# Optimization experiments

Measured on AMD Instinct MI355X. Metric: run time of the kernel, lower is better.

The kernel has to match this reference:

```python
import jax, jax.numpy as jnp
import numpy as np

N = 50000
E0 = 800000
IN_CH = 128
HID = 64
OUT_CH = 64
HEADS = 2
NEG_SLOPE = 0.2


def _xavier(key, shape):
    fan_in, fan_out = shape[-2], shape[-1]
    limit = (6.0 / (fan_in + fan_out)) ** 0.5
    return jax.random.uniform(key, shape, jnp.float32, -limit, limit)


def setup_inputs() -> dict:
    key = jax.random.key(0)
    ks = jax.random.split(key, 10)
    x = jax.random.normal(ks[0], (N, IN_CH), jnp.float32)
    src = jax.random.randint(ks[1], (E0,), 0, N)
    dst = jax.random.randint(ks[2], (E0,), 0, N)
    dst = jnp.where(src == dst, (dst + 1) % N, dst)  # no self loops in input
    edge_index = jnp.stack([src, dst]).astype(jnp.int64)
    emb_w = _xavier(ks[3], (HID, IN_CH))
    emb_b = jnp.zeros((HID,), jnp.float32)
    # layer 0: in=HID, out=HID, heads=HEADS
    w0 = _xavier(ks[4], (HEADS, HID, HID))
    a0 = _xavier(ks[5], (1, HEADS, 2 * HID))
    # layer 1: in=HEADS*HID, out=HID, heads=HEADS
    w1 = _xavier(ks[6], (HEADS, HEADS * HID, HID))
    a1 = _xavier(ks[7], (1, HEADS, 2 * HID))
    # layer 2: in=HEADS*HID, out=OUT_CH, heads=1, concat=False
    w2 = _xavier(ks[8], (1, HEADS * HID, OUT_CH))
    a2 = _xavier(ks[9], (1, 1, 2 * OUT_CH))
    return {"x": x, "edge_index": edge_index, "emb_w": emb_w, "emb_b": emb_b,
            "w0": w0, "a0": a0, "w1": w1, "a1": a1, "w2": w2, "a2": a2}


def gat_layer(x, w, a, src, dst, concat):
    # x: [N, F_in]; w: [H, F_in, C]; a: [1, H, 2C]; src/dst: [E]
    C = w.shape[-1]
    xh = jnp.einsum('nf,hfc->nhc', x, w)               # [N, H, C]
    a_i, a_j = a[0, :, :C], a[0, :, C:]                # each [H, C]
    # (cat(x_i, x_j) * a).sum(-1) == <x_i, a_i> + <x_j, a_j>; compute per node then gather
    s_i = jnp.einsum('nhc,hc->nh', xh, a_i)            # [N, H]
    s_j = jnp.einsum('nhc,hc->nh', xh, a_j)            # [N, H]
    alpha = jax.nn.leaky_relu(s_i[dst] + s_j[src], NEG_SLOPE)  # [E, H]
    # segment softmax over destination nodes
    m = jax.ops.segment_max(alpha, dst, num_segments=N)
    alpha = jnp.exp(alpha - m[dst])
    denom = jax.ops.segment_sum(alpha, dst, num_segments=N)
    alpha = alpha / (denom[dst] + 1e-16)
    out = jax.ops.segment_sum(xh[src] * alpha[:, :, None], dst, num_segments=N)  # [N, H, C]
    if concat:
        return out.reshape(N, -1)
    return out.mean(axis=1)


def _forward(x, edge_index, emb_w, emb_b, w0, a0, w1, a1, w2, a2):
    # add self loops (inputs contain none, matching remove+add in the source)
    loop = jnp.arange(N, dtype=edge_index.dtype)
    src = jnp.concatenate([edge_index[0], loop])
    dst = jnp.concatenate([edge_index[1], loop])
    h = x @ emb_w.T + emb_b                            # nn.Linear embedding
    h = jax.nn.elu(gat_layer(h, w0, a0, src, dst, True))
    h = jax.nn.elu(gat_layer(h, w1, a1, src, dst, True))
    h = jax.nn.elu(gat_layer(h, w2, a2, src, dst, False))
    return h


def reference(x, edge_index, emb_w, emb_b, w0, a0, w1, a1, w2, a2):
    return _forward(x, edge_index, emb_w, emb_b, w0, a0, w1, a1, w2, a2)
```

## Files before the change

### kernel.cpp

```cpp
#include <hip/hip_runtime.h>
#include <math.h>

typedef __attribute__((ext_vector_type(8))) short short8v;
typedef __attribute__((ext_vector_type(4))) float float4v;

union uf32 { unsigned int u; float f; };

__device__ __forceinline__ unsigned short f2b(float f) {
  uf32 v; v.f = f;
  unsigned int u = v.u;
  return (unsigned short)((u + 0x7fffu + ((u >> 16) & 1u)) >> 16);
}

__global__ void zero8(int* __restrict__ p, int n) {
  int i = blockIdx.x * 256 + threadIdx.x;
  if (i < n) p[i] = 0;
}

__global__ void hist8(const int* __restrict__ ei, int* __restrict__ cnt8,
                      unsigned short* __restrict__ lpos, int E0, int N) {
  int e = blockIdx.x * 256 + threadIdx.x;
  if (e >= E0 + N) return;
  int vx = blockIdx.x & 7;
  int d = (e < E0) ? ei[E0 + e] : (e - E0);
  lpos[e] = (unsigned short)atomicAdd(&cnt8[vx * N + d], 1);
}

__global__ void fold8(const int* __restrict__ cnt8, int* __restrict__ base8,
                      int* __restrict__ cnt, int* __restrict__ part, int N) {
  __shared__ int lds[256];
  int d = blockIdx.x * 256 + threadIdx.x;
  int run = 0;
  if (d < N) {
#pragma unroll
    for (int x = 0; x < 8; ++x) {
      int t = cnt8[x * N + d];
      base8[x * N + d] = run;
      run += t;
    }
    cnt[d] = run;
  }
  lds[threadIdx.x] = (d < N) ? run : 0;
  __syncthreads();
  for (int o = 128; o; o >>= 1) {
    if (threadIdx.x < o) lds[threadIdx.x] += lds[threadIdx.x + o];
    __syncthreads();
  }
  if (threadIdx.x == 0) part[blockIdx.x] = lds[0];
}

__global__ void scan_carry(int* __restrict__ part, int nb) {
  __shared__ int lds[256];
  __shared__ int carry;
  if (threadIdx.x == 0) carry = 0;
  __syncthreads();
  for (int t0 = 0; t0 < nb; t0 += 256) {
    int t = t0 + threadIdx.x;
    int v = (t < nb) ? part[t] : 0;
    lds[threadIdx.x] = v;
    __syncthreads();
    for (int o = 1; o < 256; o <<= 1) {
      int x = (threadIdx.x >= o) ? lds[threadIdx.x - o] : 0;
      __syncthreads();
      lds[threadIdx.x] += x;
      __syncthreads();
    }
    if (t < nb) part[t] = carry + lds[threadIdx.x] - v;
    __syncthreads();
    if (threadIdx.x == 255) carry += lds[255];
    __syncthreads();
  }
}

__global__ void scan3(const int* __restrict__ cnt, const int* __restrict__ part,
                      const int* __restrict__ base8, int* __restrict__ rp,
                      int* __restrict__ rb8, int N, int E) {
  __shared__ int lds[256];
  int t = threadIdx.x;
  int idx = blockIdx.x * 256 + t;
  int v = (idx < N) ? cnt[idx] : 0;
  lds[t] = v;
  __syncthreads();
  for (int o = 1; o < 256; o <<= 1) {
    int x = (t >= o) ? lds[t - o] : 0;
    __syncthreads();
    lds[t] += x;
    __syncthreads();
  }
  if (idx < N) {
    const int rpv = part[blockIdx.x] + lds[t] - v;
    rp[idx] = rpv;
#pragma unroll
    for (int x = 0; x < 8; ++x) rb8[x * N + idx] = rpv + base8[x * N + idx];
  }
  if (blockIdx.x == 0 && t == 0) rp[N] = E;
}

__global__ void fillx(const int* __restrict__ ei, const int* __restrict__ rb8,
                      const unsigned short* __restrict__ lpos,
                      int* __restrict__ col, int E0, int N) {
  int e = blockIdx.x * 256 + threadIdx.x;
  if (e >= E0 + N) return;
  int vx = blockIdx.x & 7;
  int s, d;
  if (e < E0) { s = ei[e]; d = ei[E0 + e]; }
  else        { s = e - E0; d = s; }
  col[rb8[vx * N + d] + lpos[e]] = s;
}

__global__ void pack_all(const float* __restrict__ emb_w, const float* __restrict__ w0,
                         const float* __restrict__ w1, const float* __restrict__ w2,
                         unsigned short* __restrict__ pE, unsigned short* __restrict__ p0,
                         unsigned short* __restrict__ p1, unsigned short* __restrict__ p2) {
  int b = blockIdx.x;
  const float* w; unsigned short* bp;
  int F, sf, sc, h;
  if (b < 32)       { w = emb_w; bp = pE; F = 128; sf = 1;  sc = 128; h = 0; }
  else if (b < 64)  { b -= 32;  w = w0; bp = p0; F = 64;  sf = 64; sc = 1; h = b / 16; b %= 16; }
  else if (b < 128) { b -= 64;  w = w1; bp = p1; F = 128; sf = 64; sc = 1; h = b / 32; b %= 32; }
  else              { b -= 128; w = w2; bp = p2; F = 128; sf = 64; sc = 1; h = 0; }
  int i = b * 256 + threadIdx.x;
  if (i >= F * 64) return;
  int j = i & 7, colc = (i >> 3) & 15, g = (i >> 7) & 3, ct = (i >> 9) & 3, kk = i >> 11;
  int f = kk * 32 + g * 8 + j;
  int c = ct * 16 + colc;
  float v = w[(size_t)h * F * 64 + (size_t)f * sf + (size_t)c * sc];
  bp[(size_t)h * F * 64 + i] = f2b(v);
}

__global__ __launch_bounds__(256) void gemm_emb_l0(
    const float* __restrict__ x, const unsigned short* __restrict__ packE,
    const float* __restrict__ emb_b, const unsigned short* __restrict__ pack0,
    const float* __restrict__ a0, unsigned short* __restrict__ xhb,
    float* __restrict__ si, float* __restrict__ sj, int nrows) {
  constexpr int SA = 136;
  constexpr int SB = 72;
  __shared__ __align__(16) unsigned short lds[64 * SA];

  const int tid = threadIdx.x;
  const int lane = tid & 63;
  const int wv = tid >> 6;
  const int n0 = blockIdx.x * 64;

#pragma unroll
  for (int i0 = 0; i0 < 64 * 32; i0 += 256) {
    const int i = i0 + tid;
    const int row = i >> 5, c4 = i & 31;
    int rg = n0 + row;
    if (rg >= nrows) rg = nrows - 1;
    const float4 v = *reinterpret_cast<const float4*>(x + (size_t)rg * 128 + c4 * 4);
    unsigned short* d = lds + row * SA + c4 * 4;
    d[0] = f2b(v.x); d[1] = f2b(v.y); d[2] = f2b(v.z); d[3] = f2b(v.w);
  }
  __syncthreads();

  const int g = lane >> 4;
  const int cl = lane & 15;

  short8v xf[4];
  {
    const unsigned short* ar = lds + (wv * 16 + cl) * SA + g * 8;
#pragma unroll
    for (int kk = 0; kk < 4; ++kk) xf[kk] = *reinterpret_cast<const short8v*>(ar + kk * 32);
  }

  float4v eacc[4];
#pragma unroll
  for (int ct = 0; ct < 4; ++ct) eacc[ct] = (float4v){0.f, 0.f, 0.f, 0.f};
#pragma unroll
  for (int kk = 0; kk < 4; ++kk) {
#pragma unroll
    for (int ct = 0; ct < 4; ++ct) {
      const short8v bf = *reinterpret_cast<const short8v*>(
          packE + ((size_t)((kk * 4 + ct) * 4 + g)) * 128 + cl * 8);
      eacc[ct] = __builtin_amdgcn_mfma_f32_16x16x32_bf16(xf[kk], bf, eacc[ct], 0, 0, 0);
    }
  }
  __syncthreads();

#pragma unroll
  for (int ct = 0; ct < 4; ++ct) {
    const float b = emb_b[ct * 16 + cl];
#pragma unroll
    for (int reg = 0; reg < 4; ++reg) {
      const int row = wv * 16 + g * 4 + reg;
      lds[row * SB + ct * 16 + cl] = f2b(eacc[ct][reg] + b);
    }
  }
  __syncthreads();

  short8v af[2];
  {
    const unsigned short* ar2 = lds + (wv * 16 + cl) * SB + g * 8;
#pragma unroll
    for (int kk = 0; kk < 2; ++kk) af[kk] = *reinterpret_cast<const short8v*>(ar2 + kk * 32);
  }

#pragma unroll
  for (int h = 0; h < 2; ++h) {
    const unsigned short* __restrict__ bph = pack0 + (size_t)h * (64 * 64);

    float4v acc[4];
#pragma unroll
    for (int ct = 0; ct < 4; ++ct) acc[ct] = (float4v){0.f, 0.f, 0.f, 0.f};
#pragma unroll
    for (int kk = 0; kk < 2; ++kk) {
#pragma unroll
      for (int ct = 0; ct < 4; ++ct) {
        const short8v bf = *reinterpret_cast<const short8v*>(
            bph + ((size_t)((kk * 4 + ct) * 4 + g)) * 128 + cl * 8);
        acc[ct] = __builtin_amdgcn_mfma_f32_16x16x32_bf16(af[kk], bf, acc[ct], 0, 0, 0);
      }
    }

#pragma unroll
    for (int ct = 0; ct < 4; ++ct) {
      const int c = ct * 16 + cl;
#pragma unroll
      for (int reg = 0; reg < 4; ++reg) {
        const int n = n0 + wv * 16 + g * 4 + reg;
        if (n < nrows) xhb[(size_t)n * 128 + h * 64 + c] = f2b(acc[ct][reg]);
      }
    }

    float pi[4] = {0.f, 0.f, 0.f, 0.f}, pj[4] = {0.f, 0.f, 0.f, 0.f};
#pragma unroll
    for (int ct = 0; ct < 4; ++ct) {
      const float av = a0[h * 128 + ct * 16 + cl];
      const float bv = a0[h * 128 + 64 + ct * 16 + cl];
#pragma unroll
      for (int reg = 0; reg < 4; ++reg) {
        pi[reg] = fmaf(acc[ct][reg], av, pi[reg]);
        pj[reg] = fmaf(acc[ct][reg], bv, pj[reg]);
      }
    }
#pragma unroll
    for (int reg = 0; reg < 4; ++reg) {
#pragma unroll
      for (int o = 8; o; o >>= 1) {
        pi[reg] += __shfl_xor(pi[reg], o, 64);
        pj[reg] += __shfl_xor(pj[reg], o, 64);
      }
    }
    if (cl == 0) {
#pragma unroll
      for (int reg = 0; reg < 4; ++reg) {
        const int n = n0 + wv * 16 + g * 4 + reg;
        if (n < nrows) {
          si[(size_t)n * 2 + h] = pi[reg];
          sj[(size_t)n * 2 + h] = pj[reg];
        }
      }
    }
  }
}

template <int F, int H, bool SCORES, bool OBF>
__global__ __launch_bounds__(256) void gemm_mfma(
    const unsigned short* __restrict__ in, const unsigned short* __restrict__ bp,
    const float* __restrict__ a, void* __restrict__ xh_out,
    float* __restrict__ si, float* __restrict__ sj, int nrows) {
  constexpr int SA = F + 8;
  constexpr int NK = F / 32;
  constexpr int HC = H * 64;
  __shared__ __align__(16) unsigned short A_lds[64 * SA];

  const int tid = threadIdx.x;
  const int lane = tid & 63;
  const int wv = tid >> 6;
  const int n0 = blockIdx.x * 64;

  {
    constexpr int NCH = 64 * F / 8;
#pragma unroll
    for (int i0 = 0; i0 < NCH; i0 += 256) {
      const int i = i0 + tid;
      const int row = i / (F / 8);
      const int c8 = i % (F / 8);
      int rg = n0 + row;
      if (rg >= nrows) rg = nrows - 1;
      const short8v v = *reinterpret_cast<const short8v*>(in + (size_t)rg * F + c8 * 8);
      *reinterpret_cast<short8v*>(A_lds + row * SA + c8 * 8) = v;
    }
  }
  __syncthreads();

  const int g = lane >> 4;
  const int cl = lane & 15;

  short8v af[NK];
  const unsigned short* ar = A_lds + (wv * 16 + cl) * SA + g * 8;
#pragma unroll
  for (int kk = 0; kk < NK; ++kk) af[kk] = *reinterpret_cast<const short8v*>(ar + kk * 32);

#pragma unroll
  for (int h = 0; h < H; ++h) {
    const unsigned short* __restrict__ bph = bp + (size_t)h * (F * 64);

    float4v acc[4];
#pragma unroll
    for (int ct = 0; ct < 4; ++ct) acc[ct] = (float4v){0.f, 0.f, 0.f, 0.f};

#pragma unroll
    for (int kk = 0; kk < NK; ++kk) {
#pragma unroll
      for (int ct = 0; ct < 4; ++ct) {
        const short8v bf = *reinterpret_cast<const short8v*>(
            bph + ((size_t)((kk * 4 + ct) * 4 + g)) * 128 + cl * 8);
        acc[ct] = __builtin_amdgcn_mfma_f32_16x16x32_bf16(af[kk], bf, acc[ct], 0, 0, 0);
      }
    }

#pragma unroll
    for (int ct = 0; ct < 4; ++ct) {
      const int c = ct * 16 + cl;
#pragma unroll
      for (int reg = 0; reg < 4; ++reg) {
        const int n = n0 + wv * 16 + g * 4 + reg;
        if (n < nrows) {
          const size_t idx = (size_t)n * HC + h * 64 + c;
          if (OBF) ((unsigned short*)xh_out)[idx] = f2b(acc[ct][reg]);
          else     ((float*)xh_out)[idx] = acc[ct][reg];
        }
      }
    }

    if (SCORES) {
      float pi[4] = {0.f, 0.f, 0.f, 0.f}, pj[4] = {0.f, 0.f, 0.f, 0.f};
#pragma unroll
      for (int ct = 0; ct < 4; ++ct) {
        const float av = a[h * 128 + ct * 16 + cl];
        const float bv = a[h * 128 + 64 + ct * 16 + cl];
#pragma unroll
        for (int reg = 0; reg < 4; ++reg) {
          pi[reg] = fmaf(acc[ct][reg], av, pi[reg]);
          pj[reg] = fmaf(acc[ct][reg], bv, pj[reg]);
        }
      }
#pragma unroll
      for (int reg = 0; reg < 4; ++reg) {
#pragma unroll
        for (int o = 8; o; o >>= 1) {
          pi[reg] += __shfl_xor(pi[reg], o, 64);
          pj[reg] += __shfl_xor(pj[reg], o, 64);
        }
      }
      if (cl == 0) {
#pragma unroll
        for (int reg = 0; reg < 4; ++reg) {
          const int n = n0 + wv * 16 + g * 4 + reg;
          if (n < nrows) {
            si[(size_t)n * H + h] = pi[reg];
            sj[(size_t)n * H + h] = pj[reg];
          }
        }
      }
    }
  }
}

template <int H, bool OBF>
__global__ __launch_bounds__(256) void agg_kernel(
    const unsigned short* __restrict__ xh, const float* __restrict__ si_g,
    const float* __restrict__ sj_g, const int* __restrict__ rp,
    const int* __restrict__ col, void* __restrict__ out, int N) {
  constexpr int HC = H * 64;
  const int lane = threadIdx.x & 63;
  const int n = blockIdx.x * 4 + (threadIdx.x >> 6);
  if (n >= N) return;
  const int el = lane & 31;
  const int hl = (H == 2) ? (lane >> 5) : 0;

  const int base = rp[n];
  const int deg = rp[n + 1] - base;
  const float siv = si_g[(size_t)n * H + hl];

  const int soff = (H == 1) ? (lane >> 5) : 0;
  const int qoff = (H == 1) ? (lane >> 5) : (lane & 32);
  constexpr int STEP = (H == 2) ? 1 : 2;
  const unsigned int loff = (H == 2) ? (unsigned)lane * 2 : (unsigned)el * 2;

  float m = 0.f, den = 0.f, acc0 = 0.f, acc1 = 0.f;

  for (int start = 0; start < deg; start += 32) {
    const int k = start + el;
    const bool vld = k < deg;
    const int s = vld ? col[base + k] : 0;
    float al = -INFINITY;
    if (vld) {
      const float t = siv + sj_g[(size_t)s * H + hl];
      al = (t > 0.f) ? t : 0.2f * t;
    }
    float cm = al;
#pragma unroll
    for (int o = 16; o; o >>= 1) cm = fmaxf(cm, __shfl_xor(cm, o, 64));
    if (start == 0) {
      m = cm;
    } else {
      const float nm = fmaxf(m, cm);
      const float r = __expf(m - nm);
      den *= r; acc0 *= r; acc1 *= r; m = nm;
    }
    const float p = vld ? __expf(al - m) : 0.f;
    float ps = p;
#pragma unroll
    for (int o = 16; o; o >>= 1) ps += __shfl_xor(ps, o, 64);
    den += ps;

    const int cc = min(32, deg - start);
    int kk = 0;
    for (; kk + 8 * STEP <= cc; kk += 8 * STEP) {
      int sb[8]; float qb[8]; unsigned int uv[8];
#pragma unroll
      for (int u = 0; u < 8; ++u) {
        const int e = kk + u * STEP;
        sb[u] = __shfl(s, e + soff, 64);
        qb[u] = __shfl(p, e + qoff, 64);
      }
#pragma unroll
      for (int u = 0; u < 8; ++u)
        uv[u] = *reinterpret_cast<const unsigned int*>(xh + (size_t)sb[u] * HC + loff);
#pragma unroll
      for (int u = 0; u < 8; ++u) {
        uf32 lo, hi;
        lo.u = uv[u] << 16;
        hi.u = uv[u] & 0xffff0000u;
        acc0 = fmaf(qb[u], lo.f, acc0);
        acc1 = fmaf(qb[u], hi.f, acc1);
      }
    }
    for (; kk + 4 * STEP <= cc; kk += 4 * STEP) {
      int sb[4]; float qb[4]; unsigned int uv[4];
#pragma unroll
      for (int u = 0; u < 4; ++u) {
        const int e = kk + u * STEP;
        sb[u] = __shfl(s, e + soff, 64);
        qb[u] = __shfl(p, e + qoff, 64);
      }
#pragma unroll
      for (int u = 0; u < 4; ++u)
        uv[u] = *reinterpret_cast<const unsigned int*>(xh + (size_t)sb[u] * HC + loff);
#pragma unroll
      for (int u = 0; u < 4; ++u) {
        uf32 lo, hi;
        lo.u = uv[u] << 16;
        hi.u = uv[u] & 0xffff0000u;
        acc0 = fmaf(qb[u], lo.f, acc0);
        acc1 = fmaf(qb[u], hi.f, acc1);
      }
    }
    for (; kk < cc; kk += STEP) {
      const int sb = __shfl(s, kk + soff, 64);
      const float qb = __shfl(p, kk + qoff, 64);
      const unsigned int uv = *reinterpret_cast<const unsigned int*>(xh + (size_t)sb * HC + loff);
      uf32 lo, hi;
      lo.u = uv << 16;
      hi.u = uv & 0xffff0000u;
      acc0 = fmaf(qb, lo.f, acc0);
      acc1 = fmaf(qb, hi.f, acc1);
    }
  }

  if (H == 2) {
    const float invd = 1.f / (den + 1e-16f);
    float v0 = acc0 * invd, v1 = acc1 * invd;
    v0 = (v0 > 0.f) ? v0 : expm1f(v0);
    v1 = (v1 > 0.f) ? v1 : expm1f(v1);
    if (OBF) {
      unsigned int pk = ((unsigned int)f2b(v1) << 16) | (unsigned int)f2b(v0);
      *reinterpret_cast<unsigned int*>((unsigned short*)out + (size_t)n * 128 + lane * 2) = pk;
    } else {
      float2 o; o.x = v0; o.y = v1;
      *reinterpret_cast<float2*>((float*)out + (size_t)n * 128 + lane * 2) = o;
    }
  } else {
    acc0 += __shfl_xor(acc0, 32, 64);
    acc1 += __shfl_xor(acc1, 32, 64);
    if (lane < 32) {
      const float invd = 1.f / (den + 1e-16f);
      float v0 = acc0 * invd, v1 = acc1 * invd;
      v0 = (v0 > 0.f) ? v0 : expm1f(v0);
      v1 = (v1 > 0.f) ? v1 : expm1f(v1);
      if (OBF) {
        unsigned int pk = ((unsigned int)f2b(v1) << 16) | (unsigned int)f2b(v0);
        *reinterpret_cast<unsigned int*>((unsigned short*)out + (size_t)n * 64 + el * 2) = pk;
      } else {
        float2 o; o.x = v0; o.y = v1;
        *reinterpret_cast<float2*>((float*)out + (size_t)n * 64 + el * 2) = o;
      }
    }
  }
}

extern "C" void kernel_launch(void* const* d_in, const int* in_sizes, int n_in,
                              void* d_out, int out_size, void* d_ws, size_t ws_size,
                              hipStream_t stream) {
  const float* x     = (const float*)d_in[0];
  const int*   ei    = (const int*)d_in[1];
  const float* emb_w = (const float*)d_in[2];
  const float* emb_b = (const float*)d_in[3];
  const float* w0    = (const float*)d_in[4];
  const float* a0    = (const float*)d_in[5];
  const float* w1    = (const float*)d_in[6];
  const float* a1    = (const float*)d_in[7];
  const float* w2    = (const float*)d_in[8];
  const float* a2    = (const float*)d_in[9];

  const int IN_CH = 128;
  int N  = in_sizes[0] / IN_CH;
  int E0 = in_sizes[1] / 2;
  int E  = E0 + N;

  char* p = (char*)d_ws;
  auto alloc = [&](size_t bytes) -> char* {
    char* r = p;
    p += (bytes + 255) & ~(size_t)255;
    return r;
  };
  unsigned short* hA  = (unsigned short*)alloc((size_t)N * 128 * 2);
  unsigned short* hB  = (unsigned short*)alloc((size_t)N * 128 * 2);
  unsigned short* xhb = (unsigned short*)alloc((size_t)N * 128 * 2);
  float* si   = (float*)alloc((size_t)N * 2 * 4);
  float* sj   = (float*)alloc((size_t)N * 2 * 4);
  unsigned short* packE = (unsigned short*)alloc(128 * 64 * 2);
  unsigned short* pack0 = (unsigned short*)alloc(2 * 64 * 64 * 2);
  unsigned short* pack1 = (unsigned short*)alloc(2 * 128 * 64 * 2);
  unsigned short* pack2 = (unsigned short*)alloc(128 * 64 * 2);
  int* rp    = (int*)alloc((size_t)(N + 1) * 4);
  int* cnt   = (int*)alloc((size_t)N * 4);
  int* cnt8  = (int*)alloc((size_t)8 * N * 4);
  int* base8 = (int*)alloc((size_t)8 * N * 4);
  int* rb8   = (int*)alloc((size_t)8 * N * 4);
  unsigned short* lpos = (unsigned short*)alloc((size_t)E * 2);
  int* col   = (int*)alloc((size_t)E * 4);
  int* part  = (int*)alloc(1024);

  dim3 blk(256);
  int gN = (N + 255) / 256;
  int gE = (E + 255) / 256;

  zero8<<<(8 * N + 255) / 256, blk, 0, stream>>>(cnt8, 8 * N);
  hist8<<<gE, blk, 0, stream>>>(ei, cnt8, lpos, E0, N);
  fold8<<<gN, blk, 0, stream>>>(cnt8, base8, cnt, part, N);
  scan_carry<<<1, blk, 0, stream>>>(part, gN);
  scan3<<<gN, blk, 0, stream>>>(cnt, part, base8, rp, rb8, N, E);
  fillx<<<gE, blk, 0, stream>>>(ei, rb8, lpos, col, E0, N);

  pack_all<<<160, blk, 0, stream>>>(emb_w, w0, w1, w2, packE, pack0, pack1, pack2);

  int gR = (N + 63) / 64;

  gemm_emb_l0<<<gR, blk, 0, stream>>>(x, packE, emb_b, pack0, a0, xhb, si, sj, N);
  agg_kernel<2, true><<<(N + 3) / 4, blk, 0, stream>>>(xhb, si, sj, rp, col, hB, N);

  gemm_mfma<128, 2, true, true><<<gR, blk, 0, stream>>>(hB, pack1, a1, xhb, si, sj, N);
  agg_kernel<2, true><<<(N + 3) / 4, blk, 0, stream>>>(xhb, si, sj, rp, col, hA, N);

  gemm_mfma<128, 1, true, true><<<gR, blk, 0, stream>>>(hA, pack2, a2, xhb, si, sj, N);
  agg_kernel<1, false><<<(N + 3) / 4, blk, 0, stream>>>(xhb, si, sj, rp, col, (float*)d_out, N);
}
```

Baseline: 201.7 us.

## Drop running softmax max and gather several edges per wave with 8-byte loads

The aggregation kernel no longer keeps a running max for the segment softmax. It takes exp of the leaky-relu score clamped at 75, and sums the denominator per lane with a single reduction at the end. This removes the per-chunk max shuffles and the rescaling of the accumulators. The gather is also reorganised so each lane loads 4 bf16 values (uint2) and half- or quarter-waves handle different edges at once, with a cross-lane reduction before the ELU and the store. The max-free exp assumes scores stay in a moderate range; very negative scores for every neighbour could underflow the denominator, and scores above 75 are clipped.

Result: no change. 205.6 us (+1.9%).

```diff
diff --git a/kernel.cpp b/kernel.cpp
--- a/kernel.cpp
+++ b/kernel.cpp
@@ -375,119 +375,96 @@
   const int deg = rp[n + 1] - base;
   const float siv = si_g[(size_t)n * H + hl];
 
-  const int soff = (H == 1) ? (lane >> 5) : 0;
-  const int qoff = (H == 1) ? (lane >> 5) : (lane & 32);
-  constexpr int STEP = (H == 2) ? 1 : 2;
-  const unsigned int loff = (H == 2) ? (unsigned)lane * 2 : (unsigned)el * 2;
-
-  float m = 0.f, den = 0.f, acc0 = 0.f, acc1 = 0.f;
+  const int egrp = (H == 2) ? (lane >> 5) : (lane >> 4);
+  constexpr int STEP = (H == 2) ? 2 : 4;
+  const int qsrc = (H == 2) ? (egrp + ((lane & 16) << 1)) : egrp;
+  const unsigned short* xrow = xh + ((H == 2) ? (unsigned)(lane & 31) * 4
+                                              : (unsigned)(lane & 15) * 4);
+
+  float den_l = 0.f;
+  float a0 = 0.f, a1 = 0.f, a2 = 0.f, a3 = 0.f;
 
   for (int start = 0; start < deg; start += 32) {
     const int k = start + el;
     const bool vld = k < deg;
     const int s = vld ? col[base + k] : 0;
-    float al = -INFINITY;
+    float p = 0.f;
     if (vld) {
       const float t = siv + sj_g[(size_t)s * H + hl];
-      al = (t > 0.f) ? t : 0.2f * t;
-    }
-    float cm = al;
-#pragma unroll
-    for (int o = 16; o; o >>= 1) cm = fmaxf(cm, __shfl_xor(cm, o, 64));
-    if (start == 0) {
-      m = cm;
-    } else {
-      const float nm = fmaxf(m, cm);
-      const float r = __expf(m - nm);
-      den *= r; acc0 *= r; acc1 *= r; m = nm;
-    }
-    const float p = vld ? __expf(al - m) : 0.f;
-    float ps = p;
-#pragma unroll
-    for (int o = 16; o; o >>= 1) ps += __shfl_xor(ps, o, 64);
-    den += ps;
+      const float al = (t > 0.f) ? t : 0.2f * t;
+      p = __expf(fminf(al, 75.f));
+    }
+    den_l += p;
 
     const int cc = min(32, deg - start);
     int kk = 0;
-    for (; kk + 8 * STEP <= cc; kk += 8 * STEP) {
-      int sb[8]; float qb[8]; unsigned int uv[8];
-#pragma unroll
-      for (int u = 0; u < 8; ++u) {
-        const int e = kk + u * STEP;
-        sb[u] = __shfl(s, e + soff, 64);
-        qb[u] = __shfl(p, e + qoff, 64);
-      }
-#pragma unroll
-      for (int u = 0; u < 8; ++u)
-        uv[u] = *reinterpret_cast<const unsigned int*>(xh + (size_t)sb[u] * HC + loff);
-#pragma unroll
-      for (int u = 0; u < 8; ++u) {
-        uf32 lo, hi;
-        lo.u = uv[u] << 16;
-        hi.u = uv[u] & 0xffff0000u;
-        acc0 = fmaf(qb[u], lo.f, acc0);
-        acc1 = fmaf(qb[u], hi.f, acc1);
-      }
-    }
     for (; kk + 4 * STEP <= cc; kk += 4 * STEP) {
-      int sb[4]; float qb[4]; unsigned int uv[4];
+      int sb[4]; float qb[4]; uint2 uv[4];
 #pragma unroll
       for (int u = 0; u < 4; ++u) {
         const int e = kk + u * STEP;
-        sb[u] = __shfl(s, e + soff, 64);
-        qb[u] = __shfl(p, e + qoff, 64);
+        sb[u] = __shfl(s, e + egrp, 64);
+        qb[u] = __shfl(p, e + qsrc, 64);
       }
 #pragma unroll
       for (int u = 0; u < 4; ++u)
-        uv[u] = *reinterpret_cast<const unsigned int*>(xh + (size_t)sb[u] * HC + loff);
+        uv[u] = *reinterpret_cast<const uint2*>(xrow + (size_t)sb[u] * HC);
 #pragma unroll
       for (int u = 0; u < 4; ++u) {
-        uf32 lo, hi;
-        lo.u = uv[u] << 16;
-        hi.u = uv[u] & 0xffff0000u;
-        acc0 = fmaf(qb[u], lo.f, acc0);
-        acc1 = fmaf(qb[u], hi.f, acc1);
+        uf32 f0, f1, f2, f3;
+        f0.u = uv[u].x << 16; f1.u = uv[u].x & 0xffff0000u;
+        f2.u = uv[u].y << 16; f3.u = uv[u].y & 0xffff0000u;
+        a0 = fmaf(qb[u], f0.f, a0);
+        a1 = fmaf(qb[u], f1.f, a1);
+        a2 = fmaf(qb[u], f2.f, a2);
+        a3 = fmaf(qb[u], f3.f, a3);
       }
     }
     for (; kk < cc; kk += STEP) {
-      const int sb = __shfl(s, kk + soff, 64);
-      const float qb = __shfl(p, kk + qoff, 64);
-      const unsigned int uv = *reinterpret_cast<const unsigned int*>(xh + (size_t)sb * HC + loff);
-      uf32 lo, hi;
-      lo.u = uv << 16;
-      hi.u = uv & 0xffff0000u;
-      acc0 = fmaf(qb, lo.f, acc0);
-      acc1 = fmaf(qb, hi.f, acc1);
-    }
-  }
-
-  if (H == 2) {
+      const int sb = __shfl(s, kk + egrp, 64);
+      const float qb = __shfl(p, kk + qsrc, 64);
+      const uint2 uv = *reinterpret_cast<const uint2*>(xrow + (size_t)sb * HC);
+      uf32 f0, f1, f2, f3;
+      f0.u = uv.x << 16; f1.u = uv.x & 0xffff0000u;
+      f2.u = uv.y << 16; f3.u = uv.y & 0xffff0000u;
+      a0 = fmaf(qb, f0.f, a0);
+      a1 = fmaf(qb, f1.f, a1);
+      a2 = fmaf(qb, f2.f, a2);
+      a3 = fmaf(qb, f3.f, a3);
+    }
+  }
+
+  a0 += __shfl_xor(a0, 32, 64);
+  a1 += __shfl_xor(a1, 32, 64);
+  a2 += __shfl_xor(a2, 32, 64);
+  a3 += __shfl_xor(a3, 32, 64);
+  if (H == 1) {
+    a0 += __shfl_xor(a0, 16, 64);
+    a1 += __shfl_xor(a1, 16, 64);
+    a2 += __shfl_xor(a2, 16, 64);
+    a3 += __shfl_xor(a3, 16, 64);
+  }
+
+#pragma unroll
+  for (int o = 16; o; o >>= 1) den_l += __shfl_xor(den_l, o, 64);
+  const float den = (H == 2) ? __shfl(den_l, (lane & 16) << 1, 64) : den_l;
+
+  const int nwrite = (H == 2) ? 32 : 16;
+  if (lane < nwrite) {
     const float invd = 1.f / (den + 1e-16f);
-    float v0 = acc0 * invd, v1 = acc1 * invd;
+    float v0 = a0 * invd, v1 = a1 * invd, v2 = a2 * invd, v3 = a3 * invd;
     v0 = (v0 > 0.f) ? v0 : expm1f(v0);
     v1 = (v1 > 0.f) ? v1 : expm1f(v1);
+    v2 = (v2 > 0.f) ? v2 : expm1f(v2);
+    v3 = (v3 > 0.f) ? v3 : expm1f(v3);
     if (OBF) {
-      unsigned int pk = ((unsigned int)f2b(v1) << 16) | (unsigned int)f2b(v0);
-      *reinterpret_cast<unsigned int*>((unsigned short*)out + (size_t)n * 128 + lane * 2) = pk;
+      uint2 pk;
+      pk.x = (unsigned int)f2b(v0) | ((unsigned int)f2b(v1) << 16);
+      pk.y = (unsigned int)f2b(v2) | ((unsigned int)f2b(v3) << 16);
+      *reinterpret_cast<uint2*>((unsigned short*)out + (size_t)n * HC + lane * 4) = pk;
     } else {
-      float2 o; o.x = v0; o.y = v1;
-      *reinterpret_cast<float2*>((float*)out + (size_t)n * 128 + lane * 2) = o;
-    }
-  } else {
-    acc0 += __shfl_xor(acc0, 32, 64);
-    acc1 += __shfl_xor(acc1, 32, 64);
-    if (lane < 32) {
-      const float invd = 1.f / (den + 1e-16f);
-      float v0 = acc0 * invd, v1 = acc1 * invd;
-      v0 = (v0 > 0.f) ? v0 : expm1f(v0);
-      v1 = (v1 > 0.f) ? v1 : expm1f(v1);
-      if (OBF) {
-        unsigned int pk = ((unsigned int)f2b(v1) << 16) | (unsigned int)f2b(v0);
-        *reinterpret_cast<unsigned int*>((unsigned short*)out + (size_t)n * 64 + el * 2) = pk;
-      } else {
-        float2 o; o.x = v0; o.y = v1;
-        *reinterpret_cast<float2*>((float*)out + (size_t)n * 64 + el * 2) = o;
-      }
+      float4 o4; o4.x = v0; o4.y = v1; o4.z = v2; o4.w = v3;
+      *reinterpret_cast<float4*>((float*)out + (size_t)n * HC + lane * 4) = o4;
     }
   }
 }
```
